# Kernel tuning notes

Hardware: AMD Instinct MI355X
Metric: run time of the kernel (lower is better)

Reference implementation:

```python
import jax, jax.numpy as jnp
import numpy as np

B, S, D, H = 4, 2048, 512, 8
DH = D // H  # depth per head = 64


def setup_inputs() -> dict:
    key = jax.random.key(0)
    ks = jax.random.split(key, 8)
    scale = 1.0 / np.sqrt(D)
    return {
        "query": jax.random.normal(ks[0], (B, S, D), jnp.float32),
        "key": jax.random.normal(ks[1], (B, S, D), jnp.float32),
        "value": jax.random.normal(ks[2], (B, S, D), jnp.float32),
        "mask": jax.random.randint(ks[3], (B, S), 0, 2, jnp.int32),
        "wq_w": jax.random.normal(ks[4], (D, D), jnp.float32) * scale,
        "wq_b": jnp.zeros((D,), jnp.float32),
        "wk_w": jax.random.normal(ks[5], (D, D), jnp.float32) * scale,
        "wk_b": jnp.zeros((D,), jnp.float32),
        "wv_w": jax.random.normal(ks[6], (D, D), jnp.float32) * scale,
        "wv_b": jnp.zeros((D,), jnp.float32),
        "wo_w": jax.random.normal(ks[7], (D, D), jnp.float32) * scale,
        "wo_b": jnp.zeros((D,), jnp.float32),
    }


def _split_heads(x):
    # [B, S, D] -> [B, H, S, DH]
    b, s, _ = x.shape
    return x.reshape(b, s, H, DH).transpose(0, 2, 1, 3)


def reference(query, key, value, mask, wq_w, wq_b, wk_w, wk_b, wv_w, wv_b, wo_w, wo_b):
    q = _split_heads(query @ wq_w + wq_b)   # [B,H,S,DH]
    k = _split_heads(key @ wk_w + wk_b)
    v = _split_heads(value @ wv_w + wv_b)

    scale = 1.0 / jnp.sqrt(jnp.asarray(DH, jnp.float32))
    logits = jnp.einsum('bhqd,bhkd->bhqk', q, k) * scale  # [B,H,S,S]
    # additive key-padding mask: 1 -> masked (adds -1e9)
    m = mask.astype(logits.dtype)[:, None, None, :]  # [B,1,1,S]
    logits = logits + m * -1e9
    weights = jax.nn.softmax(logits, axis=-1)
    attn = jnp.einsum('bhqk,bhkd->bhqd', weights, v)  # [B,H,S,DH]
    attn = attn.transpose(0, 2, 1, 3).reshape(query.shape[0], -1, D)  # [B,S,D]
    return attn @ wo_w + wo_b
```

## Files before the change

### kernel.cpp

```cpp
#include <hip/hip_runtime.h>
#include <stdint.h>

#define QSCALE (0.125f * 1.44269504088896340736f)
#define MASKNEG (-1.442695e9f)

typedef unsigned short u16;
typedef unsigned int u32;
typedef __bf16 bf16x8 __attribute__((ext_vector_type(8)));
typedef float f32x4 __attribute__((ext_vector_type(4)));
typedef float f32x16 __attribute__((ext_vector_type(16)));
typedef u16 u16x8 __attribute__((ext_vector_type(8)));
typedef u32 u32x4 __attribute__((ext_vector_type(4)));

__device__ __forceinline__ u16 f2bf(float f) {
  u32 u = __float_as_uint(f);
  u += 0x7fffu + ((u >> 16) & 1u);
  return (u16)(u >> 16);
}

__device__ __forceinline__ u32 cvtpk(float lo, float hi) {
  u32 d;
  asm("v_cvt_pk_bf16_f32 %0, %1, %2" : "=v"(d) : "v"(lo), "v"(hi));
  return d;
}

__device__ __forceinline__ void plswap(u32& a, u32& b) {
  asm("v_permlane32_swap_b32 %0, %1" : "+v"(a), "+v"(b));
}

__device__ __forceinline__ void gload16(const void* src, void* ldsbase) {
  __builtin_amdgcn_global_load_lds(
      (const __attribute__((address_space(1))) u32*)src,
      (__attribute__((address_space(3))) u32*)ldsbase, 16, 0, 0);
}

__global__ __launch_bounds__(256) void conv_w(const float* __restrict__ wq,
                                              const float* __restrict__ wk,
                                              const float* __restrict__ wv,
                                              const float* __restrict__ wo,
                                              u16* __restrict__ wT) {
  const float* src = (blockIdx.z == 0) ? wq : (blockIdx.z == 1) ? wk
                    : (blockIdx.z == 2) ? wv : wo;
  u16* dst = wT + (size_t)blockIdx.z * 262144;
  __shared__ float t[64][65];
  const int n0 = blockIdx.x * 64, k0 = blockIdx.y * 64;
  const int lr = threadIdx.x >> 6, lc = threadIdx.x & 63;
#pragma unroll
  for (int it = 0; it < 16; ++it) {
    const int row = it * 4 + lr;
    t[row][lc] = src[(size_t)(k0 + row) * 512 + n0 + lc];
  }
  __syncthreads();
#pragma unroll
  for (int it = 0; it < 16; ++it) {
    const int row = it * 4 + lr;
    dst[(size_t)(n0 + row) * 512 + k0 + lc] = f2bf(t[lc][row]);
  }
}

__global__ __launch_bounds__(256) void gemm_qkv(
    const float* __restrict__ xqf, const float* __restrict__ xkf,
    const float* __restrict__ xvf, const u16* __restrict__ wT,
    const float* __restrict__ bq, const float* __restrict__ bk,
    const float* __restrict__ bv, u16* __restrict__ qws, u16* __restrict__ kws,
    u16* __restrict__ vTw) {
  __shared__ __align__(16) char lds[65536];
  const int hw = blockIdx.x;
  const int lg = (hw & 7) * 96 + (hw >> 3);
  const int z = lg >> 8;
  const int rem = lg & 255;
  const int m0 = (rem >> 2) * 128, n0 = (rem & 3) * 128;
  const float* A = (z == 0) ? xqf : (z == 1) ? xkf : xvf;
  const u16* Bt = wT + (size_t)z * 262144;
  const float* bias = (z == 0) ? bq : (z == 1) ? bk : bv;

  const int tid = threadIdx.x;
  const int lane = tid & 63;
  const int wave = tid >> 6;
  const int wm = wave >> 1, wn = wave & 1;
  const int srow = tid >> 3;
  const int sc16 = tid & 7;

  f32x4 acc[4][4] = {};

  auto stageB = [&](int buf, int kt) {
    const int k0 = kt * 64;
    char* base = lds + buf * 32768 + 16384;
#pragma unroll
    for (int c = 0; c < 4; ++c) {
      const int row = c * 32 + srow;
      const int xc = (sc16 ^ (row & 7)) << 3;
      gload16(Bt + (size_t)(n0 + row) * 512 + k0 + xc,
              base + c * 4096 + (wave << 10));
    }
  };

  auto stageA_load = [&](int kt, float4* ld) {
    const int k0 = kt * 64;
#pragma unroll
    for (int c = 0; c < 4; ++c) {
      const int row = c * 32 + srow;
      const float* sp = A + (size_t)(m0 + row) * 512 + k0 + sc16 * 8;
      ld[c * 2] = *(const float4*)sp;
      ld[c * 2 + 1] = *(const float4*)(sp + 4);
    }
  };

  auto stageA_write = [&](int buf, const float4* ld) {
    char* base = lds + buf * 32768;
#pragma unroll
    for (int c = 0; c < 4; ++c) {
      const int row = c * 32 + srow;
      const float4 a = ld[c * 2], d = ld[c * 2 + 1];
      u16x8 w;
      w[0] = f2bf(a.x); w[1] = f2bf(a.y); w[2] = f2bf(a.z); w[3] = f2bf(a.w);
      w[4] = f2bf(d.x); w[5] = f2bf(d.y); w[6] = f2bf(d.z); w[7] = f2bf(d.w);
      *(u16x8*)(base + row * 128 + ((sc16 ^ (row & 7)) << 4)) = w;
    }
  };

  auto compute = [&](int buf) {
    const char* bA = lds + buf * 32768;
    const char* bB = bA + 16384;
#pragma unroll
    for (int kk = 0; kk < 2; ++kk) {
      const int c16 = kk * 4 + (lane >> 4);
      bf16x8 av[4], bv[4];
#pragma unroll
      for (int i = 0; i < 4; ++i) {
        const int row = wm * 64 + i * 16 + (lane & 15);
        av[i] = *(const bf16x8*)(bA + row * 128 + ((c16 ^ (row & 7)) << 4));
      }
#pragma unroll
      for (int j = 0; j < 4; ++j) {
        const int row = wn * 64 + j * 16 + (lane & 15);
        bv[j] = *(const bf16x8*)(bB + row * 128 + ((c16 ^ (row & 7)) << 4));
      }
#pragma unroll
      for (int i = 0; i < 4; ++i)
#pragma unroll
        for (int j = 0; j < 4; ++j)
          acc[i][j] = __builtin_amdgcn_mfma_f32_16x16x32_bf16(av[i], bv[j],
                                                              acc[i][j], 0, 0, 0);
    }
  };

  {
    float4 ld[8];
    stageA_load(0, ld);
    stageB(0, 0);
    stageA_write(0, ld);
  }
  __syncthreads();
#pragma unroll
  for (int kt = 0; kt < 8; ++kt) {
    const int cur = kt & 1;
    float4 nld[8];
    if (kt < 7) {
      stageA_load(kt + 1, nld);
      stageB(cur ^ 1, kt + 1);
    }
    compute(cur);
    if (kt < 7) stageA_write(cur ^ 1, nld);
    __syncthreads();
  }

#pragma unroll
  for (int j = 0; j < 4; ++j) {
    const int n = n0 + wn * 64 + j * 16 + (lane & 15);
    const float bn = bias[n];
    const int h = n >> 6, dh = n & 63;
#pragma unroll
    for (int i = 0; i < 4; ++i) {
#pragma unroll
      for (int r = 0; r < 4; ++r) {
        const int rg = m0 + wm * 64 + i * 16 + ((lane >> 4) << 2) + r;
        const int b = rg >> 11, s = rg & 2047;
        const int bh = b * 8 + h;
        const float val = acc[i][j][r] + bn;
        if (z == 0) {
          qws[((size_t)bh * 2048 + s) * 64 + dh] = f2bf(val * QSCALE);
        } else if (z == 1) {
          kws[((size_t)bh * 2048 + s) * 64 + dh] = f2bf(val);
        } else {
          vTw[((size_t)bh * 64 + dh) * 2048 + s] = f2bf(val);
        }
      }
    }
  }
}

__global__ __launch_bounds__(512, 4) void attn_fwd(
    const u16* __restrict__ qws, const u16* __restrict__ kws,
    const u16* __restrict__ vTw, const int* __restrict__ mask,
    u16* __restrict__ attn) {
  __shared__ __align__(16) char ldsK[32768];
  __shared__ __align__(16) char ldsV[32768];
  __shared__ __align__(16) float biasLDS[2048];
  __shared__ float lShA[128];

  const int bh = blockIdx.x;
  const int qt = blockIdx.y;
  const int b = bh >> 3;
  const int tid = threadIdx.x;
  const int lane = tid & 63, wave = tid >> 6;
  const int half = wave >> 2, wl = wave & 3;
  const int l31 = lane & 31, h5 = lane >> 5;

  {
    const int4 m4 = *(const int4*)(mask + b * 2048 + tid * 4);
    float4 bv;
    bv.x = m4.x ? MASKNEG : 0.0f;
    bv.y = m4.y ? MASKNEG : 0.0f;
    bv.z = m4.z ? MASKNEG : 0.0f;
    bv.w = m4.w ? MASKNEG : 0.0f;
    *(float4*)(biasLDS + tid * 4) = bv;
  }
  asm volatile("s_waitcnt lgkmcnt(0)" ::: "memory");

  const u16* qrow_p = qws + ((size_t)bh * 2048 + qt * 128 + wl * 32 + l31) * 64;
  bf16x8 qb[4];
#pragma unroll
  for (int c = 0; c < 4; ++c)
    qb[c] = *(const bf16x8*)(qrow_p + c * 16 + h5 * 8);

  const int rowb = l31 * 128;
  int kxs[4];
#pragma unroll
  for (int c = 0; c < 4; ++c) kxs[c] = ((2 * c + h5) ^ (l31 & 7)) << 4;

  char* myK = ldsK + half * 16384;
  char* myV = ldsV + half * 16384;
  const int srow = wl * 8 + (lane >> 3);
  const int sc16 = lane & 7;

  auto stage = [&](int buf, int ktg) {
#pragma unroll
    for (int c = 0; c < 2; ++c) {
      const int row = c * 32 + srow;
      const int xc = (sc16 ^ (row & 7)) << 3;
      gload16(kws + ((size_t)bh * 2048 + ktg * 64 + row) * 64 + xc,
              myK + buf * 8192 + c * 4096 + (wl << 10));
      gload16(vTw + ((size_t)bh * 64 + row) * 2048 + ktg * 64 + xc,
              myV + buf * 8192 + c * 4096 + (wl << 10));
    }
  };

  f32x16 o0 = {}, o1 = {};
  float rsp0 = 0.f, rsp1 = 0.f, rsp2 = 0.f, rsp3 = 0.f;

  auto do_subtile = [&](const char* kb, const char* vb, const float* biasT,
                        int stByte, int c0) {
    f32x16 sv;
#pragma unroll
    for (int g = 0; g < 4; ++g) {
      const f32x4 bq4 = *(const f32x4*)(biasT + g * 8 + h5 * 4);
      sv[g * 4 + 0] = bq4[0];
      sv[g * 4 + 1] = bq4[1];
      sv[g * 4 + 2] = bq4[2];
      sv[g * 4 + 3] = bq4[3];
    }
    __builtin_amdgcn_s_setprio(1);
#pragma unroll
    for (int c = 0; c < 4; ++c) {
      const bf16x8 kf = *(const bf16x8*)(kb + stByte + rowb + kxs[c]);
      sv = __builtin_amdgcn_mfma_f32_32x32x16_bf16(kf, qb[c], sv, 0, 0, 0);
    }
    __builtin_amdgcn_s_setprio(0);
    float p[16];
#pragma unroll
    for (int i = 0; i < 16; ++i) p[i] = __builtin_amdgcn_exp2f(sv[i]);
    rsp0 += p[0] + p[4] + p[8] + p[12];
    rsp1 += p[1] + p[5] + p[9] + p[13];
    rsp2 += p[2] + p[6] + p[10] + p[14];
    rsp3 += p[3] + p[7] + p[11] + p[15];
    u32 paw[2][4];
#pragma unroll
    for (int lc = 0; lc < 2; ++lc) {
      u32 a1 = cvtpk(p[lc * 8 + 0], p[lc * 8 + 1]);
      u32 b1 = cvtpk(p[lc * 8 + 4], p[lc * 8 + 5]);
      u32 a2 = cvtpk(p[lc * 8 + 2], p[lc * 8 + 3]);
      u32 b2 = cvtpk(p[lc * 8 + 6], p[lc * 8 + 7]);
      plswap(a1, b1);
      plswap(a2, b2);
      paw[lc][0] = a1; paw[lc][1] = a2; paw[lc][2] = b1; paw[lc][3] = b2;
    }
    __builtin_amdgcn_s_setprio(1);
#pragma unroll
    for (int lc = 0; lc < 2; ++lc) {
      u32x4 w = {paw[lc][0], paw[lc][1], paw[lc][2], paw[lc][3]};
      const bf16x8 pa = __builtin_bit_cast(bf16x8, w);
      const bf16x8 vf0 = *(const bf16x8*)(vb + rowb + kxs[c0 + lc]);
      o0 = __builtin_amdgcn_mfma_f32_32x32x16_bf16(pa, vf0, o0, 0, 0, 0);
      const bf16x8 vf1 = *(const bf16x8*)(vb + 4096 + rowb + kxs[c0 + lc]);
      o1 = __builtin_amdgcn_mfma_f32_32x32x16_bf16(pa, vf1, o1, 0, 0, 0);
    }
    __builtin_amdgcn_s_setprio(0);
  };

  stage(0, half * 16);

  for (int kt = 0; kt < 16; ++kt) {
    const int cur = kt & 1;
    const int ktg = half * 16 + kt;
    if (kt < 15) {
      stage(cur ^ 1, ktg + 1);
      asm volatile("s_waitcnt vmcnt(4)" ::: "memory");
    } else {
      asm volatile("s_waitcnt vmcnt(0)" ::: "memory");
    }
    __builtin_amdgcn_sched_barrier(0);
    __builtin_amdgcn_s_barrier();
    const char* kb = myK + cur * 8192;
    const char* vb = myV + cur * 8192;
    const float* biasT = biasLDS + ktg * 64;
    do_subtile(kb, vb, biasT, 0, 0);
    do_subtile(kb, vb, biasT + 32, 4096, 2);
    __builtin_amdgcn_sched_barrier(0);
    __builtin_amdgcn_s_barrier();
  }

  float rs = (rsp0 + rsp1) + (rsp2 + rsp3);
  rs += __shfl_xor(rs, 32);

  float* oSh2 = (float*)ldsK;
  u16* trb = (u16*)ldsV;
  if (half == 1) {
#pragma unroll
    for (int reg = 0; reg < 16; ++reg) {
      oSh2[(wl * 32 + reg) * 64 + lane] = o0[reg];
      oSh2[(wl * 32 + 16 + reg) * 64 + lane] = o1[reg];
    }
    if (h5 == 0) lShA[wl * 32 + l31] = rs;
  }
  __syncthreads();
  if (half == 0) {
    const float ltot = rs + lShA[wl * 32 + l31];
    const float linv = 1.0f / ltot;
#pragma unroll
    for (int reg = 0; reg < 16; ++reg) {
      const int q = (reg & 3) + 8 * (reg >> 2) + 4 * h5;
      const float inv = __shfl(linv, q);
      const float v0 = (o0[reg] + oSh2[(wl * 32 + reg) * 64 + lane]) * inv;
      const float v1 = (o1[reg] + oSh2[(wl * 32 + 16 + reg) * 64 + lane]) * inv;
      trb[(wl * 32 + q) * 64 + l31] = f2bf(v0);
      trb[(wl * 32 + q) * 64 + 32 + l31] = f2bf(v1);
    }
  }
  __syncthreads();
  const int h = bh & 7;
#pragma unroll
  for (int i = 0; i < 2; ++i) {
    const int ii = tid + i * 512;
    const int row = ii >> 3;
    const int c8 = (ii & 7) * 8;
    const u16x8 vv = *(const u16x8*)(trb + row * 64 + c8);
    const int grow = b * 2048 + qt * 128 + row;
    *(u16x8*)(attn + (size_t)grow * 512 + h * 64 + c8) = vv;
  }
}

__global__ __launch_bounds__(256) void gemm_out(const u16* __restrict__ attn,
                                                const u16* __restrict__ woT,
                                                const float* __restrict__ bo,
                                                float* __restrict__ out) {
  __shared__ __align__(16) char lds[65536];
  const int hw = blockIdx.x;
  const int lg = (hw & 7) * 32 + (hw >> 3);
  const int m0 = (lg >> 2) * 128, n0 = (lg & 3) * 128;

  const int tid = threadIdx.x;
  const int lane = tid & 63;
  const int wave = tid >> 6;
  const int wm = wave >> 1, wn = wave & 1;
  const int srow = tid >> 3;
  const int sc16 = tid & 7;

  f32x4 acc[4][4] = {};

  auto stage = [&](int buf, int kt) {
    const int k0 = kt * 64;
    char* base = lds + buf * 32768;
#pragma unroll
    for (int c = 0; c < 4; ++c) {
      const int row = c * 32 + srow;
      const int xc = (sc16 ^ (row & 7)) << 3;
      gload16(attn + (size_t)(m0 + row) * 512 + k0 + xc,
              base + c * 4096 + (wave << 10));
      gload16(woT + (size_t)(n0 + row) * 512 + k0 + xc,
              base + 16384 + c * 4096 + (wave << 10));
    }
  };

  auto compute = [&](int buf) {
    const char* bA = lds + buf * 32768;
    const char* bB = bA + 16384;
#pragma unroll
    for (int kk = 0; kk < 2; ++kk) {
      const int c16 = kk * 4 + (lane >> 4);
      bf16x8 av[4], bv[4];
#pragma unroll
      for (int i = 0; i < 4; ++i) {
        const int row = wm * 64 + i * 16 + (lane & 15);
        av[i] = *(const bf16x8*)(bA + row * 128 + ((c16 ^ (row & 7)) << 4));
      }
#pragma unroll
      for (int j = 0; j < 4; ++j) {
        const int row = wn * 64 + j * 16 + (lane & 15);
        bv[j] = *(const bf16x8*)(bB + row * 128 + ((c16 ^ (row & 7)) << 4));
      }
#pragma unroll
      for (int i = 0; i < 4; ++i)
#pragma unroll
        for (int j = 0; j < 4; ++j)
          acc[i][j] = __builtin_amdgcn_mfma_f32_16x16x32_bf16(av[i], bv[j],
                                                              acc[i][j], 0, 0, 0);
    }
  };

  stage(0, 0);
  __syncthreads();
#pragma unroll
  for (int kt = 0; kt < 8; ++kt) {
    const int cur = kt & 1;
    if (kt < 7) stage(cur ^ 1, kt + 1);
    compute(cur);
    __syncthreads();
  }

  const float bn_base = 0.f;
  (void)bn_base;
#pragma unroll
  for (int j = 0; j < 4; ++j) {
    const int n = n0 + wn * 64 + j * 16 + (lane & 15);
    const float bn = bo[n];
#pragma unroll
    for (int i = 0; i < 4; ++i) {
      const int rbase = m0 + wm * 64 + i * 16 + ((lane >> 4) << 2);
#pragma unroll
      for (int r = 0; r < 4; ++r)
        out[(size_t)(rbase + r) * 512 + n] = acc[i][j][r] + bn;
    }
  }
}

extern "C" void kernel_launch(void* const* d_in, const int* in_sizes, int n_in,
                              void* d_out, int out_size, void* d_ws,
                              size_t ws_size, hipStream_t stream) {
  (void)in_sizes; (void)n_in; (void)out_size; (void)ws_size;
  const float* q = (const float*)d_in[0];
  const float* k = (const float*)d_in[1];
  const float* v = (const float*)d_in[2];
  const int* mask = (const int*)d_in[3];
  const float* wq = (const float*)d_in[4];
  const float* bq = (const float*)d_in[5];
  const float* wk = (const float*)d_in[6];
  const float* bk = (const float*)d_in[7];
  const float* wv = (const float*)d_in[8];
  const float* bv = (const float*)d_in[9];
  const float* wo = (const float*)d_in[10];
  const float* bo = (const float*)d_in[11];

  u16* attnb = (u16*)d_ws;
  u16* wT = attnb + 3 * 4194304;
  u16* qws = wT + 1048576;
  u16* kws = qws + 4194304;
  u16* vTw = kws + 4194304;
  float* out = (float*)d_out;

  conv_w<<<dim3(8, 8, 4), 256, 0, stream>>>(wq, wk, wv, wo, wT);
  gemm_qkv<<<768, 256, 0, stream>>>(q, k, v, wT, bq, bk, bv, qws, kws, vTw);
  attn_fwd<<<dim3(32, 16), 512, 0, stream>>>(qws, kws, vTw, mask, attnb);
  gemm_out<<<256, 256, 0, stream>>>(attnb, wT + 786432, bo, out);
}
```

Measured before the change: 104.7 us.

## Deepen QKV GEMM prefetch pipeline and shrink output GEMM tiles for occupancy

The QKV projection GEMM now holds fp32 A tiles two stages ahead in registers and runs a fully unrolled schedule with explicit vmcnt waits and barriers. It also converts fp32 to bf16 with the packed v_cvt_pk_bf16_f32 instruction and sets a launch-bounds occupancy hint of 2. The output GEMM moves to 64x128 tiles with 512 blocks and less LDS, and asks for 3 blocks per CU so more waves fill the device. The workspace layout is compacted. The changes trade extra register pressure and hand-tuned wait counts for better overlap of memory and compute.

```diff
diff --git a/kernel.cpp b/kernel.cpp
--- a/kernel.cpp
+++ b/kernel.cpp
@@ -33,6 +33,23 @@
       (const __attribute__((address_space(1))) u32*)src,
       (__attribute__((address_space(3))) u32*)ldsbase, 16, 0, 0);
 }
+
+__device__ __forceinline__ u16x8 pack8(const float4& a, const float4& b) {
+  u32x4 w;
+  w[0] = cvtpk(a.x, a.y);
+  w[1] = cvtpk(a.z, a.w);
+  w[2] = cvtpk(b.x, b.y);
+  w[3] = cvtpk(b.z, b.w);
+  return __builtin_bit_cast(u16x8, w);
+}
+
+#define QKV_BAR(N)                                           \
+  do {                                                       \
+    asm volatile("s_waitcnt vmcnt(" #N ")" ::: "memory");    \
+    asm volatile("s_waitcnt lgkmcnt(0)" ::: "memory");       \
+    __builtin_amdgcn_sched_barrier(0);                       \
+    __builtin_amdgcn_s_barrier();                            \
+  } while (0)
 
 __global__ __launch_bounds__(256) void conv_w(const float* __restrict__ wq,
                                               const float* __restrict__ wk,
@@ -58,7 +75,7 @@
   }
 }
 
-__global__ __launch_bounds__(256) void gemm_qkv(
+__global__ __launch_bounds__(256, 2) void gemm_qkv(
     const float* __restrict__ xqf, const float* __restrict__ xkf,
     const float* __restrict__ xvf, const u16* __restrict__ wT,
     const float* __restrict__ bq, const float* __restrict__ bk,
@@ -82,6 +99,7 @@
   const int sc16 = tid & 7;
 
   f32x4 acc[4][4] = {};
+  float4 s0[8], s1[8];
 
   auto stageB = [&](int buf, int kt) {
     const int k0 = kt * 64;
@@ -95,7 +113,7 @@
     }
   };
 
-  auto stageA_load = [&](int kt, float4* ld) {
+  auto loadA = [&](int kt, float4* ld) {
     const int k0 = kt * 64;
 #pragma unroll
     for (int c = 0; c < 4; ++c) {
@@ -106,16 +124,13 @@
     }
   };
 
-  auto stageA_write = [&](int buf, const float4* ld) {
+  auto writeA = [&](int buf, const float4* ld) {
     char* base = lds + buf * 32768;
 #pragma unroll
     for (int c = 0; c < 4; ++c) {
       const int row = c * 32 + srow;
-      const float4 a = ld[c * 2], d = ld[c * 2 + 1];
-      u16x8 w;
-      w[0] = f2bf(a.x); w[1] = f2bf(a.y); w[2] = f2bf(a.z); w[3] = f2bf(a.w);
-      w[4] = f2bf(d.x); w[5] = f2bf(d.y); w[6] = f2bf(d.z); w[7] = f2bf(d.w);
-      *(u16x8*)(base + row * 128 + ((sc16 ^ (row & 7)) << 4)) = w;
+      *(u16x8*)(base + row * 128 + ((sc16 ^ (row & 7)) << 4)) =
+          pack8(ld[c * 2], ld[c * 2 + 1]);
     }
   };
 
@@ -145,25 +160,20 @@
     }
   };
 
-  {
-    float4 ld[8];
-    stageA_load(0, ld);
-    stageB(0, 0);
-    stageA_write(0, ld);
-  }
-  __syncthreads();
-#pragma unroll
-  for (int kt = 0; kt < 8; ++kt) {
-    const int cur = kt & 1;
-    float4 nld[8];
-    if (kt < 7) {
-      stageA_load(kt + 1, nld);
-      stageB(cur ^ 1, kt + 1);
-    }
-    compute(cur);
-    if (kt < 7) stageA_write(cur ^ 1, nld);
-    __syncthreads();
-  }
+  stageB(0, 0);
+  loadA(0, s0);
+  loadA(1, s1);
+  writeA(0, s0);
+  QKV_BAR(8);
+
+  stageB(1, 1); loadA(2, s0); writeA(1, s1); compute(0); QKV_BAR(8);
+  stageB(0, 2); loadA(3, s1); writeA(0, s0); compute(1); QKV_BAR(8);
+  stageB(1, 3); loadA(4, s0); writeA(1, s1); compute(0); QKV_BAR(8);
+  stageB(0, 4); loadA(5, s1); writeA(0, s0); compute(1); QKV_BAR(8);
+  stageB(1, 5); loadA(6, s0); writeA(1, s1); compute(0); QKV_BAR(8);
+  stageB(0, 6); loadA(7, s1); writeA(0, s0); compute(1); QKV_BAR(8);
+  stageB(1, 7);               writeA(1, s1); compute(0); QKV_BAR(0);
+                                              compute(1);
 
 #pragma unroll
   for (int j = 0; j < 4; ++j) {
@@ -360,14 +370,14 @@
   }
 }
 
-__global__ __launch_bounds__(256) void gemm_out(const u16* __restrict__ attn,
-                                                const u16* __restrict__ woT,
-                                                const float* __restrict__ bo,
-                                                float* __restrict__ out) {
-  __shared__ __align__(16) char lds[65536];
+__global__ __launch_bounds__(256, 3) void gemm_out(const u16* __restrict__ attn,
+                                                   const u16* __restrict__ woT,
+                                                   const float* __restrict__ bo,
+                                                   float* __restrict__ out) {
+  __shared__ __align__(16) char lds[49152];
   const int hw = blockIdx.x;
-  const int lg = (hw & 7) * 32 + (hw >> 3);
-  const int m0 = (lg >> 2) * 128, n0 = (lg & 3) * 128;
+  const int lg = (hw & 7) * 64 + (hw >> 3);
+  const int m0 = (lg >> 2) * 64, n0 = (lg & 3) * 128;
 
   const int tid = threadIdx.x;
   const int lane = tid & 63;
@@ -376,32 +386,37 @@
   const int srow = tid >> 3;
   const int sc16 = tid & 7;
 
-  f32x4 acc[4][4] = {};
+  f32x4 acc[2][4] = {};
 
   auto stage = [&](int buf, int kt) {
     const int k0 = kt * 64;
-    char* base = lds + buf * 32768;
-#pragma unroll
-    for (int c = 0; c < 4; ++c) {
+    char* base = lds + buf * 24576;
+#pragma unroll
+    for (int c = 0; c < 2; ++c) {
       const int row = c * 32 + srow;
       const int xc = (sc16 ^ (row & 7)) << 3;
       gload16(attn + (size_t)(m0 + row) * 512 + k0 + xc,
               base + c * 4096 + (wave << 10));
+    }
+#pragma unroll
+    for (int c = 0; c < 4; ++c) {
+      const int row = c * 32 + srow;
+      const int xc = (sc16 ^ (row & 7)) << 3;
       gload16(woT + (size_t)(n0 + row) * 512 + k0 + xc,
-              base + 16384 + c * 4096 + (wave << 10));
+              base + 8192 + c * 4096 + (wave << 10));
     }
   };
 
   auto compute = [&](int buf) {
-    const char* bA = lds + buf * 32768;
-    const char* bB = bA + 16384;
+    const char* bA = lds + buf * 24576;
+    const char* bB = bA + 8192;
 #pragma unroll
     for (int kk = 0; kk < 2; ++kk) {
       const int c16 = kk * 4 + (lane >> 4);
-      bf16x8 av[4], bv[4];
-#pragma unroll
-      for (int i = 0; i < 4; ++i) {
-        const int row = wm * 64 + i * 16 + (lane & 15);
+      bf16x8 av[2], bv[4];
+#pragma unroll
+      for (int i = 0; i < 2; ++i) {
+        const int row = wm * 32 + i * 16 + (lane & 15);
         av[i] = *(const bf16x8*)(bA + row * 128 + ((c16 ^ (row & 7)) << 4));
       }
 #pragma unroll
@@ -410,7 +425,7 @@
         bv[j] = *(const bf16x8*)(bB + row * 128 + ((c16 ^ (row & 7)) << 4));
       }
 #pragma unroll
-      for (int i = 0; i < 4; ++i)
+      for (int i = 0; i < 2; ++i)
 #pragma unroll
         for (int j = 0; j < 4; ++j)
           acc[i][j] = __builtin_amdgcn_mfma_f32_16x16x32_bf16(av[i], bv[j],
@@ -428,15 +443,13 @@
     __syncthreads();
   }
 
-  const float bn_base = 0.f;
-  (void)bn_base;
 #pragma unroll
   for (int j = 0; j < 4; ++j) {
     const int n = n0 + wn * 64 + j * 16 + (lane & 15);
     const float bn = bo[n];
 #pragma unroll
-    for (int i = 0; i < 4; ++i) {
-      const int rbase = m0 + wm * 64 + i * 16 + ((lane >> 4) << 2);
+    for (int i = 0; i < 2; ++i) {
+      const int rbase = m0 + wm * 32 + i * 16 + ((lane >> 4) << 2);
 #pragma unroll
       for (int r = 0; r < 4; ++r)
         out[(size_t)(rbase + r) * 512 + n] = acc[i][j][r] + bn;
@@ -462,7 +475,7 @@
   const float* bo = (const float*)d_in[11];
 
   u16* attnb = (u16*)d_ws;
-  u16* wT = attnb + 3 * 4194304;
+  u16* wT = attnb + 4194304;
   u16* qws = wT + 1048576;
   u16* kws = qws + 4194304;
   u16* vTw = kws + 4194304;
@@ -471,5 +484,5 @@
   conv_w<<<dim3(8, 8, 4), 256, 0, stream>>>(wq, wk, wv, wo, wT);
   gemm_qkv<<<768, 256, 0, stream>>>(q, k, v, wT, bq, bk, bv, qws, kws, vTw);
   attn_fwd<<<dim3(32, 16), 512, 0, stream>>>(qws, kws, vTw, mask, attnb);
-  gemm_out<<<256, 256, 0, stream>>>(attnb, wT + 786432, bo, out);
-}
+  gemm_out<<<512, 256, 0, stream>>>(attnb, wT + 786432, bo, out);
+}
```

After: 101.2 us. 1.03x faster.
